# Performance work log

Measured on AMD Instinct MI355X. Metric: run time of the kernel, lower is better.

## Reference

```python
import jax, jax.numpy as jnp
import numpy as np

NB_BINS = 10
N = 33554432  # 2**25 elements


def setup_inputs() -> dict:
    key = jax.random.key(0)
    k1, k2 = jax.random.split(key)
    logits = jax.random.normal(k1, (N,), dtype=jnp.float32)
    labels = jax.random.randint(k2, (N,), 0, 2, dtype=jnp.int32)
    return {"logits": logits, "labels": labels}


def reference(logits, labels):
    # confidences in (0,1); bins are (l, u] over linspace(0,1,nb+1),
    # so bin index = ceil(conf * nb) - 1, clipped to [0, nb-1].
    conf = jax.nn.sigmoid(logits)
    idx = jnp.clip(jnp.ceil(conf * NB_BINS).astype(jnp.int32) - 1, 0, NB_BINS - 1)

    counts = jax.ops.segment_sum(jnp.ones_like(conf), idx, num_segments=NB_BINS)
    sum_conf = jax.ops.segment_sum(conf, idx, num_segments=NB_BINS)
    sum_pos = jax.ops.segment_sum(labels.astype(conf.dtype), idx, num_segments=NB_BINS)

    denom = jnp.maximum(counts, 1.0)
    nonempty = counts > 0
    positives_per_bin = jnp.where(nonempty, sum_pos / denom, 0.0)
    confidence_per_bin = jnp.where(nonempty, sum_conf / denom, 0.0)
    return jnp.stack([positives_per_bin, confidence_per_bin])  # [2, nb_bins]
```

## Files before the change

kernel.cpp:

```cpp
#include <hip/hip_runtime.h>

typedef unsigned int u32;
typedef unsigned long long u64;

#define NB 10
#define BLOCKS 2048
#define TPB 256
#define ITERS 8
#define CHUNK_F4 128
#define WAVE_F4 (ITERS * CHUNK_F4)

typedef __attribute__((address_space(3))) char lds_char;
typedef __attribute__((address_space(1))) const char g_char;

__device__ __forceinline__ void dma16(const void* g, void* l) {
    __builtin_amdgcn_global_load_lds((g_char*)g, (lds_char*)l, 16, 0, 0);
}

#define WAIT_VM(nn)  __builtin_amdgcn_s_waitcnt(((nn) & 15) | 0xF70)
#define WAIT_LGKM0() __builtin_amdgcn_s_waitcnt(0xC07F)

#if defined(__has_builtin)
#if __has_builtin(__builtin_amdgcn_sched_barrier)
#define SCHEDB() __builtin_amdgcn_sched_barrier(0)
#else
#define SCHEDB()
#endif
#else
#define SCHEDB()
#endif

__global__ void rd_zero_ws(u32* __restrict__ ws) {
    if (threadIdx.x < 320) ws[threadIdx.x] = 0u;
}

__device__ __forceinline__ void rd_acc(float x, int lab,
                                       u64& c64, u64& p64, u64& flo, u64& fhi) {
    float e = __expf(-x);
    float conf = __builtin_amdgcn_rcpf(1.0f + e);
    float t10 = __builtin_fmaf(conf, 10.0f, -1e-6f);
    int b = min(9, (int)t10);
    float frac = t10 - (float)b;
    u32 ffx = (u32)__builtin_fmaf(frac, 127.0f, 0.5f);

    u32 sh6 = (u32)(b * 6);
    c64 += 1ull << sh6;
    p64 += ((u64)(u32)lab) << sh6;

    bool lo = b < 5;
    u32 sh12 = (u32)(b * 12);
    u32 shf = lo ? sh12 : (sh12 - 60u);
    u64 v = ((u64)ffx) << shf;
    flo += lo ? v : 0ull;
    fhi += lo ? 0ull : v;
}

__device__ __forceinline__ void rd_acc4(const float4& x, const int4& y,
                                        u64& c64, u64& p64, u64& flo, u64& fhi) {
    rd_acc(x.x, y.x, c64, p64, flo, fhi);
    rd_acc(x.y, y.y, c64, p64, flo, fhi);
    rd_acc(x.z, y.z, c64, p64, flo, fhi);
    rd_acc(x.w, y.w, c64, p64, flo, fhi);
}

__global__ __launch_bounds__(TPB) void rd_hist(const float* __restrict__ logits,
                                               const int* __restrict__ labels,
                                               u32* __restrict__ ws,
                                               long long n) {
    __shared__ __align__(16) char lds[32 * 1024];

    u32 cp[NB], cf[NB];
    #pragma unroll
    for (int b = 0; b < NB; ++b) { cp[b] = 0u; cf[b] = 0u; }

    const float4* l4 = (const float4*)logits;
    const int4*   i4 = (const int4*)labels;
    int lane = threadIdx.x & 63;
    int wave = threadIdx.x >> 6;
    long long nf4 = n >> 2;
    long long seg = (long long)blockIdx.x * (4 * WAVE_F4);

    if (seg + 4 * WAVE_F4 <= nf4) {
        long long gb = seg + (long long)wave * WAVE_F4;
        const float4* gl = l4 + gb + lane;
        const int4*   gi = i4 + gb + lane;
        char* myl = lds + wave * 8192;

        #define ISSUE(t, bb) do {                               \
            char* _base = myl + (bb) * 4096;                    \
            dma16(gl + (t) * CHUNK_F4,      _base);             \
            dma16(gl + (t) * CHUNK_F4 + 64, _base + 1024);      \
            dma16(gi + (t) * CHUNK_F4,      _base + 2048);      \
            dma16(gi + (t) * CHUNK_F4 + 64, _base + 3072);      \
        } while (0)

        ISSUE(0, 0);
        ISSUE(1, 1);

        u64 c64 = 0, p64 = 0, flo = 0, fhi = 0;
        #pragma unroll
        for (int t = 0; t < ITERS; ++t) {
            const int bb = t & 1;
            const char* base = myl + bb * 4096;
            if (t < ITERS - 1) { WAIT_VM(4); } else { WAIT_VM(0); }
            SCHEDB();
            float4 xa = *(const float4*)(base + lane * 16);
            float4 xb = *(const float4*)(base + 1024 + lane * 16);
            int4   ya = *(const int4*)(base + 2048 + lane * 16);
            int4   yb = *(const int4*)(base + 3072 + lane * 16);
            WAIT_LGKM0();
            SCHEDB();
            if (t + 2 < ITERS) ISSUE(t + 2, bb);
            SCHEDB();
            rd_acc4(xa, ya, c64, p64, flo, fhi);
            rd_acc4(xb, yb, c64, p64, flo, fhi);
            if ((t & 3) == 3) {
                #pragma unroll
                for (int b = 0; b < NB; ++b) {
                    u32 cnt = (u32)(c64 >> (6 * b)) & 63u;
                    u32 pos = (u32)(p64 >> (6 * b)) & 63u;
                    cp[b] += cnt | (pos << 16);
                    cf[b] += (b < 5) ? ((u32)(flo >> (12 * b)) & 4095u)
                                     : ((u32)(fhi >> (12 * (b - 5))) & 4095u);
                }
                c64 = 0; p64 = 0; flo = 0; fhi = 0;
            }
        }
        #undef ISSUE
    }

    long long done_f4 = ((long long)gridDim.x < nf4 / (4 * WAVE_F4)
                             ? (long long)gridDim.x
                             : nf4 / (4 * WAVE_F4)) * (4 * WAVE_F4);
    long long tail = done_f4 * 4;
    if (tail < n) {
        long long tid    = (long long)blockIdx.x * blockDim.x + threadIdx.x;
        long long stride = (long long)gridDim.x * blockDim.x;
        for (long long i = tail + tid; i < n; i += stride) {
            float e = __expf(-logits[i]);
            float conf = __builtin_amdgcn_rcpf(1.0f + e);
            float t10 = __builtin_fmaf(conf, 10.0f, -1e-6f);
            int b = min(9, (int)t10);
            float frac = t10 - (float)b;
            u32 ffx = (u32)__builtin_fmaf(frac, 127.0f, 0.5f);
            atomicAdd((u64*)&ws[32 * b], (u64)ffx);
            atomicAdd(&ws[32 * b + 2], 1u);
            atomicAdd(&ws[32 * b + 3], (u32)labels[i]);
        }
    }

    __shared__ u32 s_cp[4][NB];
    __shared__ u32 s_cf[4][NB];
    #pragma unroll
    for (int b = 0; b < NB; ++b) {
        u32 c = cp[b];
        u32 f = cf[b];
        #pragma unroll
        for (int off = 32; off; off >>= 1) {
            c += __shfl_down(c, off, 64);
            f += __shfl_down(f, off, 64);
        }
        if (lane == 0) { s_cp[wave][b] = c; s_cf[wave][b] = f; }
    }
    __syncthreads();

    if (threadIdx.x < NB) {
        int b = threadIdx.x;
        u32 c = s_cp[0][b] + s_cp[1][b] + s_cp[2][b] + s_cp[3][b];
        u64 f = (u64)s_cf[0][b] + s_cf[1][b] + s_cf[2][b] + s_cf[3][b];
        atomicAdd((u64*)&ws[32 * b], f);
        atomicAdd(&ws[32 * b + 2], c & 0xFFFFu);
        atomicAdd(&ws[32 * b + 3], c >> 16);
    }
}

__global__ void rd_finalize(const u32* __restrict__ ws, float* __restrict__ out) {
    int b = threadIdx.x;
    if (b < NB) {
        u64 f   = *(const u64*)&ws[32 * b];
        u32 cnt = ws[32 * b + 2];
        u32 pos = ws[32 * b + 3];
        double sumconf = ((double)b * (double)cnt + (double)f * (1.0 / 127.0)) * 0.1;
        float denom = fmaxf((float)cnt, 1.0f);
        bool ne = cnt > 0u;
        out[b]      = ne ? ((float)pos / denom) : 0.0f;
        out[NB + b] = ne ? (float)(sumconf / (double)denom) : 0.0f;
    }
}

extern "C" void kernel_launch(void* const* d_in, const int* in_sizes, int n_in,
                              void* d_out, int out_size, void* d_ws, size_t ws_size,
                              hipStream_t stream) {
    const float* logits = (const float*)d_in[0];
    const int*   labels = (const int*)d_in[1];
    float* out = (float*)d_out;
    u32*   ws  = (u32*)d_ws;
    long long n = (long long)in_sizes[0];

    rd_zero_ws<<<1, 512, 0, stream>>>(ws);
    rd_hist<<<BLOCKS, TPB, 0, stream>>>(logits, labels, ws, n);
    rd_finalize<<<1, 64, 0, stream>>>(ws, out);
}
```

Measured before the change: 293.8 us.

## Replace LDS DMA double-buffered pipeline with direct grid-stride vector loads

Removes the global_load_lds double-buffering scheme and its waitcnt and sched_barrier scheduling. Each thread now issues four float4 and four int4 global loads per iteration in a grid-stride loop over 4096 blocks, and the tail is handled with the same packed register accumulators instead of global atomics. The aim is to drop the LDS round-trip and the fixed segment mapping, and to let more blocks and outstanding loads hide memory latency. The cost is losing the explicit prefetch overlap, and the tail now uses a scalar path.

```diff
diff --git a/kernel.cpp b/kernel.cpp
--- a/kernel.cpp
+++ b/kernel.cpp
@@ -4,31 +4,8 @@
 typedef unsigned long long u64;
 
 #define NB 10
-#define BLOCKS 2048
+#define BLOCKS 4096
 #define TPB 256
-#define ITERS 8
-#define CHUNK_F4 128
-#define WAVE_F4 (ITERS * CHUNK_F4)
-
-typedef __attribute__((address_space(3))) char lds_char;
-typedef __attribute__((address_space(1))) const char g_char;
-
-__device__ __forceinline__ void dma16(const void* g, void* l) {
-    __builtin_amdgcn_global_load_lds((g_char*)g, (lds_char*)l, 16, 0, 0);
-}
-
-#define WAIT_VM(nn)  __builtin_amdgcn_s_waitcnt(((nn) & 15) | 0xF70)
-#define WAIT_LGKM0() __builtin_amdgcn_s_waitcnt(0xC07F)
-
-#if defined(__has_builtin)
-#if __has_builtin(__builtin_amdgcn_sched_barrier)
-#define SCHEDB() __builtin_amdgcn_sched_barrier(0)
-#else
-#define SCHEDB()
-#endif
-#else
-#define SCHEDB()
-#endif
 
 __global__ void rd_zero_ws(u32* __restrict__ ws) {
     if (threadIdx.x < 320) ws[threadIdx.x] = 0u;
@@ -67,90 +44,67 @@
                                                const int* __restrict__ labels,
                                                u32* __restrict__ ws,
                                                long long n) {
-    __shared__ __align__(16) char lds[32 * 1024];
-
     u32 cp[NB], cf[NB];
     #pragma unroll
     for (int b = 0; b < NB; ++b) { cp[b] = 0u; cf[b] = 0u; }
 
     const float4* l4 = (const float4*)logits;
     const int4*   i4 = (const int4*)labels;
+    long long nf4 = n >> 2;
+    long long tid = (long long)blockIdx.x * TPB + threadIdx.x;
+    long long stride = (long long)gridDim.x * TPB;
+
+    u64 c64 = 0, p64 = 0, flo = 0, fhi = 0;
+    int pend = 0;
+
+    #define UNPACK() do {                                                   \
+        _Pragma("unroll")                                                   \
+        for (int b = 0; b < NB; ++b) {                                      \
+            u32 cnt = (u32)(c64 >> (6 * b)) & 63u;                          \
+            u32 pos = (u32)(p64 >> (6 * b)) & 63u;                          \
+            cp[b] += cnt | (pos << 16);                                     \
+            cf[b] += (b < 5) ? ((u32)(flo >> (12 * b)) & 4095u)             \
+                             : ((u32)(fhi >> (12 * (b - 5))) & 4095u);      \
+        }                                                                   \
+        c64 = 0; p64 = 0; flo = 0; fhi = 0;                                 \
+    } while (0)
+
+    long long i = tid;
+    for (; i + 3 * stride < nf4; i += 4 * stride) {
+        float4 x0 = l4[i];
+        float4 x1 = l4[i + stride];
+        float4 x2 = l4[i + 2 * stride];
+        float4 x3 = l4[i + 3 * stride];
+        int4   y0 = i4[i];
+        int4   y1 = i4[i + stride];
+        int4   y2 = i4[i + 2 * stride];
+        int4   y3 = i4[i + 3 * stride];
+        rd_acc4(x0, y0, c64, p64, flo, fhi);
+        rd_acc4(x1, y1, c64, p64, flo, fhi);
+        rd_acc4(x2, y2, c64, p64, flo, fhi);
+        rd_acc4(x3, y3, c64, p64, flo, fhi);
+        pend += 16;
+        if (pend == 32) { UNPACK(); pend = 0; }
+    }
+    for (; i < nf4; i += stride) {
+        float4 x = l4[i];
+        int4   y = i4[i];
+        rd_acc4(x, y, c64, p64, flo, fhi);
+        pend += 4;
+        if (pend == 32) { UNPACK(); pend = 0; }
+    }
+    long long base = nf4 << 2;
+    for (long long j = base + tid; j < n; j += stride) {
+        rd_acc(logits[j], labels[j], c64, p64, flo, fhi);
+        if (++pend == 32) { UNPACK(); pend = 0; }
+    }
+    if (pend) UNPACK();
+    #undef UNPACK
+
+    __shared__ u32 s_cp[TPB / 64][NB];
+    __shared__ u32 s_cf[TPB / 64][NB];
     int lane = threadIdx.x & 63;
     int wave = threadIdx.x >> 6;
-    long long nf4 = n >> 2;
-    long long seg = (long long)blockIdx.x * (4 * WAVE_F4);
-
-    if (seg + 4 * WAVE_F4 <= nf4) {
-        long long gb = seg + (long long)wave * WAVE_F4;
-        const float4* gl = l4 + gb + lane;
-        const int4*   gi = i4 + gb + lane;
-        char* myl = lds + wave * 8192;
-
-        #define ISSUE(t, bb) do {                               \
-            char* _base = myl + (bb) * 4096;                    \
-            dma16(gl + (t) * CHUNK_F4,      _base);             \
-            dma16(gl + (t) * CHUNK_F4 + 64, _base + 1024);      \
-            dma16(gi + (t) * CHUNK_F4,      _base + 2048);      \
-            dma16(gi + (t) * CHUNK_F4 + 64, _base + 3072);      \
-        } while (0)
-
-        ISSUE(0, 0);
-        ISSUE(1, 1);
-
-        u64 c64 = 0, p64 = 0, flo = 0, fhi = 0;
-        #pragma unroll
-        for (int t = 0; t < ITERS; ++t) {
-            const int bb = t & 1;
-            const char* base = myl + bb * 4096;
-            if (t < ITERS - 1) { WAIT_VM(4); } else { WAIT_VM(0); }
-            SCHEDB();
-            float4 xa = *(const float4*)(base + lane * 16);
-            float4 xb = *(const float4*)(base + 1024 + lane * 16);
-            int4   ya = *(const int4*)(base + 2048 + lane * 16);
-            int4   yb = *(const int4*)(base + 3072 + lane * 16);
-            WAIT_LGKM0();
-            SCHEDB();
-            if (t + 2 < ITERS) ISSUE(t + 2, bb);
-            SCHEDB();
-            rd_acc4(xa, ya, c64, p64, flo, fhi);
-            rd_acc4(xb, yb, c64, p64, flo, fhi);
-            if ((t & 3) == 3) {
-                #pragma unroll
-                for (int b = 0; b < NB; ++b) {
-                    u32 cnt = (u32)(c64 >> (6 * b)) & 63u;
-                    u32 pos = (u32)(p64 >> (6 * b)) & 63u;
-                    cp[b] += cnt | (pos << 16);
-                    cf[b] += (b < 5) ? ((u32)(flo >> (12 * b)) & 4095u)
-                                     : ((u32)(fhi >> (12 * (b - 5))) & 4095u);
-                }
-                c64 = 0; p64 = 0; flo = 0; fhi = 0;
-            }
-        }
-        #undef ISSUE
-    }
-
-    long long done_f4 = ((long long)gridDim.x < nf4 / (4 * WAVE_F4)
-                             ? (long long)gridDim.x
-                             : nf4 / (4 * WAVE_F4)) * (4 * WAVE_F4);
-    long long tail = done_f4 * 4;
-    if (tail < n) {
-        long long tid    = (long long)blockIdx.x * blockDim.x + threadIdx.x;
-        long long stride = (long long)gridDim.x * blockDim.x;
-        for (long long i = tail + tid; i < n; i += stride) {
-            float e = __expf(-logits[i]);
-            float conf = __builtin_amdgcn_rcpf(1.0f + e);
-            float t10 = __builtin_fmaf(conf, 10.0f, -1e-6f);
-            int b = min(9, (int)t10);
-            float frac = t10 - (float)b;
-            u32 ffx = (u32)__builtin_fmaf(frac, 127.0f, 0.5f);
-            atomicAdd((u64*)&ws[32 * b], (u64)ffx);
-            atomicAdd(&ws[32 * b + 2], 1u);
-            atomicAdd(&ws[32 * b + 3], (u32)labels[i]);
-        }
-    }
-
-    __shared__ u32 s_cp[4][NB];
-    __shared__ u32 s_cf[4][NB];
     #pragma unroll
     for (int b = 0; b < NB; ++b) {
         u32 c = cp[b];
@@ -166,8 +120,9 @@
 
     if (threadIdx.x < NB) {
         int b = threadIdx.x;
-        u32 c = s_cp[0][b] + s_cp[1][b] + s_cp[2][b] + s_cp[3][b];
-        u64 f = (u64)s_cf[0][b] + s_cf[1][b] + s_cf[2][b] + s_cf[3][b];
+        u32 c = 0; u64 f = 0;
+        #pragma unroll
+        for (int w = 0; w < TPB / 64; ++w) { c += s_cp[w][b]; f += s_cf[w][b]; }
         atomicAdd((u64*)&ws[32 * b], f);
         atomicAdd(&ws[32 * b + 2], c & 0xFFFFu);
         atomicAdd(&ws[32 * b + 3], c >> 16);
```

Result: slower. 345.7 us (+17.6%).
